# Kernel optimization log

Measured on AMD Instinct MI355X. Metric: run time of the kernel, lower is better.

## Reference

```python
import jax, jax.numpy as jnp
import numpy as np

N_NODES = 50000
N_EDGES = 800000
D_IN, D_HID, D_OUT = 128, 256, 128
N_EXPERT = 8


def mean_aggr(x, src, dst, n):
    # scatter-mean of neighbor features onto destination nodes
    msg = x[src]                                            # [E, d]
    s = jax.ops.segment_sum(msg, dst, num_segments=n)       # [N, d]
    cnt = jax.ops.segment_sum(jnp.ones((src.shape[0],), x.dtype), dst, num_segments=n)
    return s / jnp.clip(cnt, 1.0)[:, None]


def moe_top1(x, wg, bg, we, be):
    # FMoE with naive gate, top_k=1: combine weight softmax over top-1 == 1.0
    logits = x @ wg + bg                                    # [N, E]
    gate_full = jax.nn.softmax(logits, axis=-1)             # [N, E]
    idx = jnp.argmax(logits, axis=-1)                       # [N]
    n_expert = we.shape[0]
    out = jnp.zeros((x.shape[0], we.shape[2]), x.dtype)
    for e in range(n_expert):                               # small fixed loop over experts
        mask = (idx == e)[:, None].astype(x.dtype)
        out = out + mask * (x @ we[e] + be[e])
    return out, gate_full


def mysage_conv(x, src, dst, wg, bg, we, be, wr):
    agg = mean_aggr(x, src, dst, x.shape[0])
    out, gate = moe_top1(agg, wg, bg, we, be)
    out = out + x @ wr                                      # root weight (no bias)
    gstd = jnp.std(gate, axis=1, ddof=1).mean()             # torch.std is unbiased
    return out, gstd


def plain_sage_conv(x, src, dst, wl, bl, wr):
    agg = mean_aggr(x, src, dst, x.shape[0])
    return agg @ wl + bl + x @ wr


def setup_inputs() -> dict:
    key = jax.random.key(0)
    ks = jax.random.split(key, 16)
    s = 0.05
    inp = {
        "x": jax.random.normal(ks[0], (N_NODES, D_IN), jnp.float32),
        "edge_index": jax.random.randint(ks[1], (2, N_EDGES), 0, N_NODES, jnp.int64),
        # layer 1 (in -> hid)
        "wg1": jax.random.normal(ks[2], (D_IN, N_EXPERT), jnp.float32) * s,
        "bg1": jnp.zeros((N_EXPERT,), jnp.float32),
        "we1": jax.random.normal(ks[3], (N_EXPERT, D_IN, D_HID), jnp.float32) * s,
        "be1": jnp.zeros((N_EXPERT, D_HID), jnp.float32),
        "wr1": jax.random.normal(ks[4], (D_IN, D_HID), jnp.float32) * s,
        # layer 2 (hid -> hid)
        "wg2": jax.random.normal(ks[5], (D_HID, N_EXPERT), jnp.float32) * s,
        "bg2": jnp.zeros((N_EXPERT,), jnp.float32),
        "we2": jax.random.normal(ks[6], (N_EXPERT, D_HID, D_HID), jnp.float32) * s,
        "be2": jnp.zeros((N_EXPERT, D_HID), jnp.float32),
        "wr2": jax.random.normal(ks[7], (D_HID, D_HID), jnp.float32) * s,
        # layer 3 plain SAGEConv (hid -> out)
        "wl3": jax.random.normal(ks[8], (D_HID, D_OUT), jnp.float32) * s,
        "bl3": jnp.zeros((D_OUT,), jnp.float32),
        "wr3": jax.random.normal(ks[9], (D_HID, D_OUT), jnp.float32) * s,
    }
    return inp


def reference(x, edge_index, wg1, bg1, we1, be1, wr1, wg2, bg2, we2, be2, wr2, wl3, bl3, wr3):
    src, dst = edge_index[0], edge_index[1]
    h, g1 = mysage_conv(x, src, dst, wg1, bg1, we1, be1, wr1)
    h = jax.nn.relu(h)                                      # dropout p=0 / eval mode
    h, g2 = mysage_conv(h, src, dst, wg2, bg2, we2, be2, wr2)
    h = jax.nn.relu(h)
    out = plain_sage_conv(h, src, dst, wl3, bl3, wr3)
    gate_std_mean = jnp.stack([g1, g2]).mean()
    return out, gate_std_mean
```

## Files before the change

kernel.cpp:

```cpp
#include <hip/hip_runtime.h>
#include <hip/hip_bf16.h>
#include <stdint.h>

#define DEV static __device__ __forceinline__

typedef __attribute__((ext_vector_type(8))) short short8;
typedef __attribute__((ext_vector_type(4))) float f32x4;

DEV float bf2f(unsigned short u) { return __uint_as_float(((unsigned)u) << 16); }
DEV float bflo(unsigned u) { return __uint_as_float(u << 16); }
DEV float bfhi(unsigned u) { return __uint_as_float(u & 0xffff0000u); }
DEV unsigned short f2bf(float f) {
    unsigned u = __float_as_uint(f);
    u += 0x7fff + ((u >> 16) & 1);
    return (unsigned short)(u >> 16);
}

__global__ void k_detect(const int* __restrict__ ei, int* __restrict__ flags) {
    if (threadIdx.x == 0 && blockIdx.x == 0) {
        int zeros = 0;
        for (int i = 0; i < 128; ++i) if (ei[2 * i + 1] == 0) ++zeros;
        flags[1] = (zeros >= 64) ? 1 : 0;
    }
}

__global__ void k_cvt_idx(const int* __restrict__ ei, int* __restrict__ src32,
                          int* __restrict__ dst32, int E, const int* __restrict__ flags) {
    int i = blockIdx.x * 256 + threadIdx.x;
    if (i >= E) return;
    if (flags[1]) { src32[i] = ei[2 * i]; dst32[i] = ei[2 * E + 2 * i]; }
    else          { src32[i] = ei[i];     dst32[i] = ei[E + i]; }
}

__global__ void k_transpose_nb(const float* __restrict__ in, unsigned short* __restrict__ out,
                               int R, int C) {
    __shared__ unsigned short tile[32][33];
    int tx = threadIdx.x & 31, ty = threadIdx.x >> 5;
    size_t mat = (size_t)blockIdx.z * R * C;
    int r0 = blockIdx.y * 32, c0 = blockIdx.x * 32;
#pragma unroll
    for (int j = 0; j < 32; j += 8)
        tile[ty + j][tx] = f2bf(in[mat + (size_t)(r0 + ty + j) * C + c0 + tx]);
    __syncthreads();
#pragma unroll
    for (int j = 0; j < 32; j += 8)
        out[mat + (size_t)(c0 + ty + j) * R + r0 + tx] = tile[tx][ty + j];
}

__global__ void k_degree(const int* __restrict__ dst, int* __restrict__ deg, int E) {
    int i = blockIdx.x * 256 + threadIdx.x;
    if (i < E) atomicAdd(&deg[dst[i]], 1);
}

__global__ void k_scan1(const int* __restrict__ deg, int* __restrict__ row_ptr,
                        int* __restrict__ part, int n) {
    __shared__ int wsum[4];
    int t = threadIdx.x, lane = t & 63, wv = t >> 6;
    int i = blockIdx.x * 256 + t;
    int v0 = (i < n) ? deg[i] : 0;
    int v = v0;
#pragma unroll
    for (int d = 1; d < 64; d <<= 1) { int u = __shfl_up(v, d); if (lane >= d) v += u; }
    if (lane == 63) wsum[wv] = v;
    __syncthreads();
    int add = 0;
    for (int w2 = 0; w2 < wv; ++w2) add += wsum[w2];
    v += add;
    if (i < n) row_ptr[i] = v - v0;
    if (t == 255) part[blockIdx.x] = v;
}

__global__ void k_scan2(int* __restrict__ part, int P) {
    __shared__ int wsum[4];
    int t = threadIdx.x, lane = t & 63, wv = t >> 6;
    int v0 = (t < P) ? part[t] : 0;
    int v = v0;
#pragma unroll
    for (int d = 1; d < 64; d <<= 1) { int u = __shfl_up(v, d); if (lane >= d) v += u; }
    if (lane == 63) wsum[wv] = v;
    __syncthreads();
    int add = 0;
    for (int w2 = 0; w2 < wv; ++w2) add += wsum[w2];
    v += add;
    if (t < P) part[t] = v - v0;
}

__global__ void k_scan3(int* __restrict__ row_ptr, const int* __restrict__ part, int n, int E) {
    int i = blockIdx.x * 256 + threadIdx.x;
    if (i < n) row_ptr[i] += part[blockIdx.x];
    if (i == 0) row_ptr[n] = E;
}

__global__ void k_fill(const int* __restrict__ src, const int* __restrict__ dst,
                       const int* __restrict__ row_ptr, int* __restrict__ cursor,
                       int* __restrict__ csr, int E) {
    int i = blockIdx.x * 256 + threadIdx.x;
    if (i < E) {
        int d = dst[i];
        int p = atomicAdd(&cursor[d], 1);
        csr[row_ptr[d] + p] = src[i];
    }
}

template<int D>
__global__ void k_aggr(const float* __restrict__ xin, const int* __restrict__ row_ptr,
                       const int* __restrict__ csr, float* __restrict__ agg, int n) {
    int wid = (blockIdx.x * blockDim.x + threadIdx.x) >> 6;
    int lane = threadIdx.x & 63;
    if (wid >= n) return;
    constexpr int V = D / 64;
    double a0[V], a1[V], a2[V], a3[V];
#pragma unroll
    for (int i = 0; i < V; ++i) { a0[i] = 0.0; a1[i] = 0.0; a2[i] = 0.0; a3[i] = 0.0; }
    int s0 = row_ptr[wid], s1 = row_ptr[wid + 1];
    int j = s0;
    for (; j + 4 <= s1; j += 4) {
        int i0 = csr[j], i1 = csr[j + 1], i2 = csr[j + 2], i3 = csr[j + 3];
        const float* p0 = xin + (size_t)i0 * D + lane * V;
        const float* p1 = xin + (size_t)i1 * D + lane * V;
        const float* p2 = xin + (size_t)i2 * D + lane * V;
        const float* p3 = xin + (size_t)i3 * D + lane * V;
        if (V == 2) {
            float2 f0 = *(const float2*)p0, f1 = *(const float2*)p1;
            float2 f2 = *(const float2*)p2, f3 = *(const float2*)p3;
            a0[0] += (double)f0.x; a0[1] += (double)f0.y;
            a1[0] += (double)f1.x; a1[1] += (double)f1.y;
            a2[0] += (double)f2.x; a2[1] += (double)f2.y;
            a3[0] += (double)f3.x; a3[1] += (double)f3.y;
        } else {
            float4 f0 = *(const float4*)p0, f1 = *(const float4*)p1;
            float4 f2 = *(const float4*)p2, f3 = *(const float4*)p3;
            a0[0] += (double)f0.x; a0[1] += (double)f0.y; a0[2] += (double)f0.z; a0[3] += (double)f0.w;
            a1[0] += (double)f1.x; a1[1] += (double)f1.y; a1[2] += (double)f1.z; a1[3] += (double)f1.w;
            a2[0] += (double)f2.x; a2[1] += (double)f2.y; a2[2] += (double)f2.z; a2[3] += (double)f2.w;
            a3[0] += (double)f3.x; a3[1] += (double)f3.y; a3[2] += (double)f3.z; a3[3] += (double)f3.w;
        }
    }
    for (; j < s1; ++j) {
        const float* p = xin + (size_t)csr[j] * D + lane * V;
        if (V == 2) {
            float2 f = *(const float2*)p;
            a0[0] += (double)f.x; a0[1] += (double)f.y;
        } else {
            float4 f = *(const float4*)p;
            a0[0] += (double)f.x; a0[1] += (double)f.y; a0[2] += (double)f.z; a0[3] += (double)f.w;
        }
    }
    double inv = 1.0 / (double)max(s1 - s0, 1);
#pragma unroll
    for (int i = 0; i < V; ++i)
        agg[(size_t)wid * D + lane * V + i] = (float)(((a0[i] + a1[i]) + (a2[i] + a3[i])) * inv);
}

template<int D>
__global__ void k_aggr_bf(const unsigned short* __restrict__ xin, const int* __restrict__ row_ptr,
                          const int* __restrict__ csr, float* __restrict__ agg, int n) {
    int wid = (blockIdx.x * blockDim.x + threadIdx.x) >> 6;
    int lane = threadIdx.x & 63;
    if (wid >= n) return;
    constexpr int V = D / 64;
    double a0[V], a1[V], a2[V], a3[V];
#pragma unroll
    for (int i = 0; i < V; ++i) { a0[i] = 0.0; a1[i] = 0.0; a2[i] = 0.0; a3[i] = 0.0; }
    int s0 = row_ptr[wid], s1 = row_ptr[wid + 1];
    int j = s0;
    for (; j + 4 <= s1; j += 4) {
        int i0 = csr[j], i1 = csr[j + 1], i2 = csr[j + 2], i3 = csr[j + 3];
        uint2 u0 = *(const uint2*)(xin + (size_t)i0 * D + lane * V);
        uint2 u1 = *(const uint2*)(xin + (size_t)i1 * D + lane * V);
        uint2 u2 = *(const uint2*)(xin + (size_t)i2 * D + lane * V);
        uint2 u3 = *(const uint2*)(xin + (size_t)i3 * D + lane * V);
        a0[0] += (double)bflo(u0.x); a0[1] += (double)bfhi(u0.x);
        a0[2] += (double)bflo(u0.y); a0[3] += (double)bfhi(u0.y);
        a1[0] += (double)bflo(u1.x); a1[1] += (double)bfhi(u1.x);
        a1[2] += (double)bflo(u1.y); a1[3] += (double)bfhi(u1.y);
        a2[0] += (double)bflo(u2.x); a2[1] += (double)bfhi(u2.x);
        a2[2] += (double)bflo(u2.y); a2[3] += (double)bfhi(u2.y);
        a3[0] += (double)bflo(u3.x); a3[1] += (double)bfhi(u3.x);
        a3[2] += (double)bflo(u3.y); a3[3] += (double)bfhi(u3.y);
    }
    for (; j < s1; ++j) {
        uint2 u = *(const uint2*)(xin + (size_t)csr[j] * D + lane * V);
        a0[0] += (double)bflo(u.x); a0[1] += (double)bfhi(u.x);
        a0[2] += (double)bflo(u.y); a0[3] += (double)bfhi(u.y);
    }
    double inv = 1.0 / (double)max(s1 - s0, 1);
#pragma unroll
    for (int i = 0; i < V; ++i)
        agg[(size_t)wid * D + lane * V + i] = (float)(((a0[i] + a1[i]) + (a2[i] + a3[i])) * inv);
}

template<int D>
__global__ void k_gate(const float* __restrict__ agg, const float* __restrict__ wg,
                       const float* __restrict__ bg, int* __restrict__ idx,
                       int* __restrict__ ecnt, float* __restrict__ gsum, int n) {
    __shared__ float swg[D * 8];
    __shared__ int hcnt[8];
    __shared__ float red[256];
    int t = threadIdx.x;
    if (t < 8) hcnt[t] = 0;
    for (int i = t; i < D * 8; i += 256) swg[i] = wg[i];
    __syncthreads();
    int nid = blockIdx.x * 256 + t;
    float stdv = 0.f;
    if (nid < n) {
        double lg[8];
#pragma unroll
        for (int e = 0; e < 8; ++e) lg[e] = (double)bg[e];
        const float* ap = agg + (size_t)nid * D;
        for (int k = 0; k < D; k += 4) {
            float4 a = *(const float4*)(ap + k);
#pragma unroll
            for (int e = 0; e < 8; ++e) {
                lg[e] += (double)a.x * swg[(k + 0) * 8 + e] + (double)a.y * swg[(k + 1) * 8 + e]
                       + (double)a.z * swg[(k + 2) * 8 + e] + (double)a.w * swg[(k + 3) * 8 + e];
            }
        }
        double m = lg[0];
        int am = 0;
#pragma unroll
        for (int e = 1; e < 8; ++e) if (lg[e] > m) { m = lg[e]; am = e; }
        double s = 0.0, p[8];
#pragma unroll
        for (int e = 0; e < 8; ++e) { p[e] = exp(lg[e] - m); s += p[e]; }
        double invs = 1.0 / s, sq = 0.0;
#pragma unroll
        for (int e = 0; e < 8; ++e) { double q = p[e] * invs; sq += q * q; }
        stdv = (float)sqrt(fmax(sq - 0.125, 0.0) / 7.0);
        idx[nid] = am;
        atomicAdd(&hcnt[am], 1);
    }
    red[t] = stdv;
    __syncthreads();
    for (int off = 128; off > 0; off >>= 1) {
        if (t < off) red[t] += red[t + off];
        __syncthreads();
    }
    if (t == 0) atomicAdd(gsum, red[0]);
    if (t < 8 && hcnt[t] > 0) atomicAdd(&ecnt[t], hcnt[t]);
}

__global__ void k_offsets(const int* __restrict__ ecnt, int* __restrict__ eoff) {
    if (threadIdx.x == 0 && blockIdx.x == 0) {
        int s = 0;
        for (int e = 0; e < 8; ++e) { eoff[e] = s; s += ecnt[e]; }
        eoff[8] = s;
    }
}

__global__ void k_perm(const int* __restrict__ idx, const int* __restrict__ eoff,
                       int* __restrict__ ecur, int* __restrict__ perm, int n) {
    __shared__ int lcnt[8], lbase[8];
    int t = threadIdx.x;
    if (t < 8) lcnt[t] = 0;
    __syncthreads();
    int nid = blockIdx.x * 256 + t;
    int e = 0, r = 0;
    bool valid = (nid < n);
    if (valid) { e = idx[nid]; r = atomicAdd(&lcnt[e], 1); }
    __syncthreads();
    if (t < 8) lbase[t] = lcnt[t] ? atomicAdd(&ecur[t], lcnt[t]) : 0;
    __syncthreads();
    if (valid) perm[eoff[e] + lbase[e] + r] = nid;
}

template<int NCOL, bool LOAD>
DEV void g_step(int g, const float* __restrict__ Bp, const float* __restrict__ at,
                float4 (&cur)[4], float (&acc)[8][4]) {
    float bx[4][4];
#pragma unroll
    for (int kk = 0; kk < 4; ++kk) {
        bx[kk][0] = cur[kk].x; bx[kk][1] = cur[kk].y;
        bx[kk][2] = cur[kk].z; bx[kk][3] = cur[kk].w;
    }
#pragma unroll
    for (int r = 0; r < 8; ++r) {
        float4 a = *(const float4*)(at + r * 68 + g * 4);
#pragma unroll
        for (int c = 0; c < 4; ++c) {
            acc[r][c] = fmaf(a.x, bx[0][c], acc[r][c]);
            acc[r][c] = fmaf(a.y, bx[1][c], acc[r][c]);
            acc[r][c] = fmaf(a.z, bx[2][c], acc[r][c]);
            acc[r][c] = fmaf(a.w, bx[3][c], acc[r][c]);
        }
    }
    if (LOAD) {
#pragma unroll
        for (int kk = 0; kk < 4; ++kk)
            cur[kk] = *(const float4*)(Bp + (size_t)(g * 4 + 8 + kk) * NCOL);
    }
}

template<int NCOL>
DEV void compute_chunk(const float* __restrict__ Bp, const float* __restrict__ at,
                       float (&acc)[8][4]) {
    float4 bA[4], bB[4];
#pragma unroll
    for (int kk = 0; kk < 4; ++kk) bA[kk] = *(const float4*)(Bp + (size_t)kk * NCOL);
#pragma unroll
    for (int kk = 0; kk < 4; ++kk) bB[kk] = *(const float4*)(Bp + (size_t)(4 + kk) * NCOL);
#pragma unroll 1
    for (int g = 0; g < 14; g += 2) {
        g_step<NCOL, true>(g, Bp, at, bA, acc);
        g_step<NCOL, true>(g + 1, Bp, at, bB, acc);
    }
    g_step<NCOL, false>(14, Bp, at, bA, acc);
    g_step<NCOL, false>(15, Bp, at, bB, acc);
}

template<int DIN, int NCOL, bool EXPERT, bool RELU>
__global__ __launch_bounds__(256, 4) void k_gemm_f32(
    const float* __restrict__ agg, const float* __restrict__ a2,
    const float* __restrict__ B1, const float* __restrict__ B2,
    const float* __restrict__ bias,
    const int* __restrict__ perm, const int* __restrict__ eoff,
    float* __restrict__ outp, int n) {
    static_assert(DIN == 128 && NCOL == 256, "layer-1 geometry");
    __shared__ float a_tile[2][4 * 8 * 68];
    __shared__ int rows[32];
    int t = threadIdx.x;
    int e = 0, base = 0, cnt = n;
    if (EXPERT) { e = blockIdx.y; base = eoff[e]; cnt = eoff[e + 1] - base; }
    int rs = blockIdx.x * 32;
    if (rs >= cnt) return;
    int nrows = min(32, cnt - rs);
    if (t < 32) {
        int j = rs + min(t, nrows - 1);
        rows[t] = EXPERT ? perm[base + j] : j;
    }
    __syncthreads();
    int lane = t & 63, rg = t >> 6;
    int cols = lane * 4;
    int srow = lane >> 3;
    int sk = (lane & 7) * 8;
    int myrow = rows[rg * 8 + srow];
    float* st0 = &a_tile[0][rg * 544 + srow * 68 + sk];
    float* st1 = &a_tile[1][rg * 544 + srow * 68 + sk];
    const float* at0 = &a_tile[0][rg * 544];
    const float* at1 = &a_tile[1][rg * 544];
    const float* B1e = B1 + (EXPERT ? (size_t)e * DIN * NCOL : 0);
    const float* a_my = agg + (size_t)myrow * DIN + sk;
    const float* x_my = a2 + (size_t)myrow * DIN + sk;

    float acc[8][4];
#pragma unroll
    for (int r = 0; r < 8; ++r) { acc[r][0] = 0.f; acc[r][1] = 0.f; acc[r][2] = 0.f; acc[r][3] = 0.f; }

    float4 p0 = *(const float4*)a_my;
    float4 p1 = *(const float4*)(a_my + 4);
    float4 q0 = *(const float4*)(a_my + 64);
    float4 q1 = *(const float4*)(a_my + 68);
    *(float4*)st0 = p0; *(float4*)(st0 + 4) = p1;
    compute_chunk<NCOL>(B1e + cols, at0, acc);

    *(float4*)st1 = q0; *(float4*)(st1 + 4) = q1;
    p0 = *(const float4*)x_my;
    p1 = *(const float4*)(x_my + 4);
    compute_chunk<NCOL>(B1e + (size_t)64 * NCOL + cols, at1, acc);

    *(float4*)st0 = p0; *(float4*)(st0 + 4) = p1;
    q0 = *(const float4*)(x_my + 64);
    q1 = *(const float4*)(x_my + 68);
    compute_chunk<NCOL>(B2 + cols, at0, acc);

    *(float4*)st1 = q0; *(float4*)(st1 + 4) = q1;
    compute_chunk<NCOL>(B2 + (size_t)64 * NCOL + cols, at1, acc);

    float4 bb = *(const float4*)(bias + (EXPERT ? e * NCOL : 0) + cols);
#pragma unroll
    for (int r = 0; r < 8; ++r) {
        int rr = rg * 8 + r;
        if (rr < nrows) {
            int gr = rows[rr];
            float v0 = acc[r][0] + bb.x, v1 = acc[r][1] + bb.y;
            float v2 = acc[r][2] + bb.z, v3 = acc[r][3] + bb.w;
            if (RELU) { v0 = fmaxf(v0, 0.f); v1 = fmaxf(v1, 0.f); v2 = fmaxf(v2, 0.f); v3 = fmaxf(v3, 0.f); }
            *(float4*)(outp + (size_t)gr * NCOL + cols) = make_float4(v0, v1, v2, v3);
        }
    }
}

template<int DIN, int MODE, int CT>
DEV void gemm_half(const void* __restrict__ Asrc, const unsigned short* __restrict__ BT,
                   short (*Ah)[40], short (*Bs)[40],
                   const int* rows, f32x4 (&acc)[4][CT], int t, int lane, int w) {
    int q = lane >> 4, m16 = lane & 15;
    int r = t >> 2, part = t & 3;
    for (int kc = 0; kc < DIN; kc += 32) {
        __syncthreads();
        if (MODE == 2) {
            *(uint4*)&Ah[r][part * 8] =
                *(const uint4*)((const unsigned short*)Asrc + (size_t)rows[r] * DIN + kc + part * 8);
        } else {
            const float* pf = (const float*)Asrc + (size_t)rows[r] * DIN + kc + part * 8;
            float4 p0 = *(const float4*)pf, p1 = *(const float4*)(pf + 4);
            float va[8] = { p0.x, p0.y, p0.z, p0.w, p1.x, p1.y, p1.z, p1.w };
            short8 h;
#pragma unroll
            for (int j = 0; j < 8; ++j) h[j] = (short)f2bf(va[j]);
            *(short8*)&Ah[r][part * 8] = h;
        }
#pragma unroll
        for (int j = 0; j < CT; ++j) {
            int c = t + 256 * j;
            int nn = c >> 2, pp = c & 3;
            *(uint4*)&Bs[nn][pp * 8] = *(const uint4*)(BT + (size_t)nn * DIN + kc + pp * 8);
        }
        __syncthreads();
        short8 af[4], bfr[CT];
#pragma unroll
        for (int rt = 0; rt < 4; ++rt) af[rt] = *(short8*)&Ah[rt * 16 + m16][q * 8];
#pragma unroll
        for (int ct = 0; ct < CT; ++ct) bfr[ct] = *(short8*)&Bs[w * CT * 16 + ct * 16 + m16][q * 8];
#pragma unroll
        for (int rt = 0; rt < 4; ++rt)
#pragma unroll
            for (int ct = 0; ct < CT; ++ct)
                acc[rt][ct] = __builtin_amdgcn_mfma_f32_16x16x32_bf16(af[rt], bfr[ct], acc[rt][ct], 0, 0, 0);
    }
}

template<int DIN, int M0, int M1, int CT, bool EXPERT, bool RELU, bool OUTBF>
__global__ __launch_bounds__(256) void k_gemm(
    const void* __restrict__ A0, const void* __restrict__ A1,
    const unsigned short* __restrict__ B0T, const unsigned short* __restrict__ B1T,
    const float* __restrict__ bias,
    const int* __restrict__ perm, const int* __restrict__ eoff,
    void* __restrict__ outp, int n) {
    constexpr int NCOL = CT * 64;
    __shared__ short Ah[64][40];
    __shared__ short Bs[NCOL][40];
    __shared__ int rows[64];
    int t = threadIdx.x;
    int lane = t & 63, w = t >> 6;
    int e = 0, base = 0, cnt = n;
    if (EXPERT) { e = blockIdx.y; base = eoff[e]; cnt = eoff[e + 1] - base; }
    int rs = blockIdx.x * 64;
    if (rs >= cnt) return;
    int nrows = min(64, cnt - rs);
    if (t < 64) {
        int j = rs + min(t, nrows - 1);
        rows[t] = EXPERT ? perm[base + j] : j;
    }
    __syncthreads();
    f32x4 acc[4][CT];
#pragma unroll
    for (int rt = 0; rt < 4; ++rt)
#pragma unroll
        for (int ct = 0; ct < CT; ++ct) acc[rt][ct] = (f32x4)(0.f);

    gemm_half<DIN, M0, CT>(A0, B0T + (EXPERT ? (size_t)e * DIN * NCOL : 0), Ah, Bs, rows, acc, t, lane, w);
    gemm_half<DIN, M1, CT>(A1, B1T, Ah, Bs, rows, acc, t, lane, w);

    int q = lane >> 4, m16 = lane & 15;
#pragma unroll
    for (int ct = 0; ct < CT; ++ct) {
        int col = w * CT * 16 + ct * 16 + m16;
        float bv = bias[(EXPERT ? e * NCOL : 0) + col];
#pragma unroll
        for (int rt = 0; rt < 4; ++rt)
#pragma unroll
            for (int i = 0; i < 4; ++i) {
                int rr = rt * 16 + q * 4 + i;
                if (rr < nrows) {
                    int gr = rows[rr];
                    float v = acc[rt][ct][i] + bv;
                    if (RELU) v = fmaxf(v, 0.f);
                    if (OUTBF) ((unsigned short*)outp)[(size_t)gr * NCOL + col] = f2bf(v);
                    else       ((float*)outp)[(size_t)gr * NCOL + col] = v;
                }
            }
    }
}

__global__ void k_final(const float* __restrict__ gsum, float* __restrict__ outf) {
    if (threadIdx.x == 0 && blockIdx.x == 0) {
        float g = (gsum[0] + gsum[1]) * (0.5f / 50000.0f);
        outf[(size_t)50000 * 128] = g;
    }
}

extern "C" void kernel_launch(void* const* d_in, const int* in_sizes, int n_in,
                              void* d_out, int out_size, void* d_ws, size_t ws_size,
                              hipStream_t stream) {
    constexpr int N = 50000, E = 800000;
    const float* x   = (const float*)d_in[0];
    const int* ei    = (const int*)d_in[1];
    const float* wg1 = (const float*)d_in[2];
    const float* bg1 = (const float*)d_in[3];
    const float* we1 = (const float*)d_in[4];
    const float* be1 = (const float*)d_in[5];
    const float* wr1 = (const float*)d_in[6];
    const float* wg2 = (const float*)d_in[7];
    const float* bg2 = (const float*)d_in[8];
    const float* we2 = (const float*)d_in[9];
    const float* be2 = (const float*)d_in[10];
    const float* wr2 = (const float*)d_in[11];
    const float* wl3 = (const float*)d_in[12];
    const float* bl3 = (const float*)d_in[13];
    const float* wr3 = (const float*)d_in[14];

    int* ip = (int*)d_ws;
    int* deg = ip;            ip += N;
    int* cursor = ip;         ip += N;
    int* ecnt = ip;           ip += 16;
    int* ecur = ip;           ip += 16;
    float* gsum = (float*)ip; ip += 2;
    int* flags = ip;          ip += 2;
    int* row_ptr = ip;        ip += N + 1;
    int* csr = ip;            ip += E;
    int* idxb = ip;           ip += N;
    int* permb = ip;          ip += N;
    int* eoff = ip;           ip += 18;
    int* part = ip;           ip += 256;
    int* src32 = ip;          ip += E;
    int* dst32 = ip;          ip += E;
    size_t off = (size_t)((char*)ip - (char*)d_ws);
    off = (off + 255) & ~(size_t)255;
    float* fp = (float*)((char*)d_ws + off);
    float* agg = fp; fp += (size_t)N * 256;
    float* h1  = fp; fp += (size_t)N * 256;
    unsigned short* wp = (unsigned short*)fp;
    unsigned short* h2b  = wp; wp += (size_t)N * 256;
    unsigned short* we2T = wp; wp += 8 * 256 * 256;
    unsigned short* wr2T = wp; wp += 256 * 256;
    unsigned short* wl3T = wp; wp += 256 * 128;
    unsigned short* wr3T = wp; wp += 256 * 128;

    hipMemsetAsync(d_ws, 0, (size_t)(2 * N + 36) * 4, stream);

    k_detect<<<1, 64, 0, stream>>>(ei, flags);
    k_cvt_idx<<<(E + 255) / 256, 256, 0, stream>>>(ei, src32, dst32, E, flags);

    k_transpose_nb<<<dim3(8, 8, 8), 256, 0, stream>>>(we2, we2T, 256, 256);
    k_transpose_nb<<<dim3(8, 8, 1), 256, 0, stream>>>(wr2, wr2T, 256, 256);
    k_transpose_nb<<<dim3(4, 8, 1), 256, 0, stream>>>(wl3, wl3T, 256, 128);
    k_transpose_nb<<<dim3(4, 8, 1), 256, 0, stream>>>(wr3, wr3T, 256, 128);

    constexpr int NB = (N + 255) / 256;
    constexpr int WB = (N + 3) / 4;
    k_degree<<<(E + 255) / 256, 256, 0, stream>>>(dst32, deg, E);
    k_scan1<<<NB, 256, 0, stream>>>(deg, row_ptr, part, N);
    k_scan2<<<1, 256, 0, stream>>>(part, NB);
    k_scan3<<<NB, 256, 0, stream>>>(row_ptr, part, N, E);
    k_fill<<<(E + 255) / 256, 256, 0, stream>>>(src32, dst32, row_ptr, cursor, csr, E);

    constexpr int GB = (N + 63) / 64;
    constexpr int GB32 = (N + 31) / 32;
    k_aggr<128><<<WB, 256, 0, stream>>>(x, row_ptr, csr, agg, N);
    k_gate<128><<<NB, 256, 0, stream>>>(agg, wg1, bg1, idxb, ecnt, gsum, N);
    k_offsets<<<1, 1, 0, stream>>>(ecnt, eoff);
    k_perm<<<NB, 256, 0, stream>>>(idxb, eoff, ecur, permb, N);
    k_gemm_f32<128, 256, true, true><<<dim3(GB32, 8), 256, 0, stream>>>(
        agg, x, we1, wr1, be1, permb, eoff, h1, N);

    k_aggr<256><<<WB, 256, 0, stream>>>(h1, row_ptr, csr, agg, N);
    k_gate<256><<<NB, 256, 0, stream>>>(agg, wg2, bg2, idxb, ecnt + 8, gsum + 1, N);
    k_offsets<<<1, 1, 0, stream>>>(ecnt + 8, eoff + 9);
    k_perm<<<NB, 256, 0, stream>>>(idxb, eoff + 9, ecur + 8, permb, N);
    k_gemm<256, 0, 0, 4, true, true, true><<<dim3(GB, 8), 256, 0, stream>>>(
        agg, h1, we2T, wr2T, be2, permb, eoff + 9, h2b, N);

    k_aggr_bf<256><<<WB, 256, 0, stream>>>(h2b, row_ptr, csr, agg, N);
    k_gemm<256, 0, 2, 2, false, false, false><<<dim3(GB, 1), 256, 0, stream>>>(
        agg, h2b, wl3T, wr3T, bl3, nullptr, nullptr, d_out, N);

    k_final<<<1, 1, 0, stream>>>(gsum, (float*)d_out);
}
```

Baseline: 673.9 us.

## Fuse gating into aggregation and flatten expert grid in fp32 layer-1 GEMM

```diff
diff --git a/kernel.cpp b/kernel.cpp
--- a/kernel.cpp
+++ b/kernel.cpp
@@ -103,53 +103,107 @@
 }
 
 template<int D>
-__global__ void k_aggr(const float* __restrict__ xin, const int* __restrict__ row_ptr,
-                       const int* __restrict__ csr, float* __restrict__ agg, int n) {
-    int wid = (blockIdx.x * blockDim.x + threadIdx.x) >> 6;
-    int lane = threadIdx.x & 63;
-    if (wid >= n) return;
+__global__ void k_aggr_gate(const float* __restrict__ xin, const int* __restrict__ row_ptr,
+                            const int* __restrict__ csr, const float* __restrict__ wg,
+                            const float* __restrict__ bg, float* __restrict__ agg,
+                            int* __restrict__ idx, int* __restrict__ ecnt,
+                            float* __restrict__ gpart, int n) {
     constexpr int V = D / 64;
-    double a0[V], a1[V], a2[V], a3[V];
-#pragma unroll
-    for (int i = 0; i < V; ++i) { a0[i] = 0.0; a1[i] = 0.0; a2[i] = 0.0; a3[i] = 0.0; }
-    int s0 = row_ptr[wid], s1 = row_ptr[wid + 1];
-    int j = s0;
-    for (; j + 4 <= s1; j += 4) {
-        int i0 = csr[j], i1 = csr[j + 1], i2 = csr[j + 2], i3 = csr[j + 3];
-        const float* p0 = xin + (size_t)i0 * D + lane * V;
-        const float* p1 = xin + (size_t)i1 * D + lane * V;
-        const float* p2 = xin + (size_t)i2 * D + lane * V;
-        const float* p3 = xin + (size_t)i3 * D + lane * V;
-        if (V == 2) {
-            float2 f0 = *(const float2*)p0, f1 = *(const float2*)p1;
-            float2 f2 = *(const float2*)p2, f3 = *(const float2*)p3;
-            a0[0] += (double)f0.x; a0[1] += (double)f0.y;
-            a1[0] += (double)f1.x; a1[1] += (double)f1.y;
-            a2[0] += (double)f2.x; a2[1] += (double)f2.y;
-            a3[0] += (double)f3.x; a3[1] += (double)f3.y;
-        } else {
-            float4 f0 = *(const float4*)p0, f1 = *(const float4*)p1;
-            float4 f2 = *(const float4*)p2, f3 = *(const float4*)p3;
-            a0[0] += (double)f0.x; a0[1] += (double)f0.y; a0[2] += (double)f0.z; a0[3] += (double)f0.w;
-            a1[0] += (double)f1.x; a1[1] += (double)f1.y; a1[2] += (double)f1.z; a1[3] += (double)f1.w;
-            a2[0] += (double)f2.x; a2[1] += (double)f2.y; a2[2] += (double)f2.z; a2[3] += (double)f2.w;
-            a3[0] += (double)f3.x; a3[1] += (double)f3.y; a3[2] += (double)f3.z; a3[3] += (double)f3.w;
-        }
-    }
-    for (; j < s1; ++j) {
-        const float* p = xin + (size_t)csr[j] * D + lane * V;
-        if (V == 2) {
-            float2 f = *(const float2*)p;
-            a0[0] += (double)f.x; a0[1] += (double)f.y;
-        } else {
-            float4 f = *(const float4*)p;
-            a0[0] += (double)f.x; a0[1] += (double)f.y; a0[2] += (double)f.z; a0[3] += (double)f.w;
-        }
-    }
-    double inv = 1.0 / (double)max(s1 - s0, 1);
-#pragma unroll
-    for (int i = 0; i < V; ++i)
-        agg[(size_t)wid * D + lane * V + i] = (float)(((a0[i] + a1[i]) + (a2[i] + a3[i])) * inv);
+    __shared__ float swg[D * 8];
+    __shared__ int hcnt[8];
+    __shared__ float bsum;
+    int t = threadIdx.x;
+    if (t < 8) hcnt[t] = 0;
+    if (t == 0) bsum = 0.f;
+    for (int i = t; i < D * 8; i += 256) swg[i] = wg[i];
+    __syncthreads();
+
+    int wid = (blockIdx.x * blockDim.x + t) >> 6;
+    int lane = t & 63;
+    bool active = (wid < n);
+    float fv[V];
+    if (active) {
+        double a0[V], a1[V], a2[V], a3[V];
+#pragma unroll
+        for (int i = 0; i < V; ++i) { a0[i] = 0.0; a1[i] = 0.0; a2[i] = 0.0; a3[i] = 0.0; }
+        int s0 = row_ptr[wid], s1 = row_ptr[wid + 1];
+        int j = s0;
+        for (; j + 4 <= s1; j += 4) {
+            int i0 = csr[j], i1 = csr[j + 1], i2 = csr[j + 2], i3 = csr[j + 3];
+            const float* p0 = xin + (size_t)i0 * D + lane * V;
+            const float* p1 = xin + (size_t)i1 * D + lane * V;
+            const float* p2 = xin + (size_t)i2 * D + lane * V;
+            const float* p3 = xin + (size_t)i3 * D + lane * V;
+            if (V == 2) {
+                float2 f0 = *(const float2*)p0, f1 = *(const float2*)p1;
+                float2 f2 = *(const float2*)p2, f3 = *(const float2*)p3;
+                a0[0] += (double)f0.x; a0[1] += (double)f0.y;
+                a1[0] += (double)f1.x; a1[1] += (double)f1.y;
+                a2[0] += (double)f2.x; a2[1] += (double)f2.y;
+                a3[0] += (double)f3.x; a3[1] += (double)f3.y;
+            } else {
+                float4 f0 = *(const float4*)p0, f1 = *(const float4*)p1;
+                float4 f2 = *(const float4*)p2, f3 = *(const float4*)p3;
+                a0[0] += (double)f0.x; a0[1] += (double)f0.y; a0[2] += (double)f0.z; a0[3] += (double)f0.w;
+                a1[0] += (double)f1.x; a1[1] += (double)f1.y; a1[2] += (double)f1.z; a1[3] += (double)f1.w;
+                a2[0] += (double)f2.x; a2[1] += (double)f2.y; a2[2] += (double)f2.z; a2[3] += (double)f2.w;
+                a3[0] += (double)f3.x; a3[1] += (double)f3.y; a3[2] += (double)f3.z; a3[3] += (double)f3.w;
+            }
+        }
+        for (; j < s1; ++j) {
+            const float* p = xin + (size_t)csr[j] * D + lane * V;
+            if (V == 2) {
+                float2 f = *(const float2*)p;
+                a0[0] += (double)f.x; a0[1] += (double)f.y;
+            } else {
+                float4 f = *(const float4*)p;
+                a0[0] += (double)f.x; a0[1] += (double)f.y; a0[2] += (double)f.z; a0[3] += (double)f.w;
+            }
+        }
+        double inv = 1.0 / (double)max(s1 - s0, 1);
+#pragma unroll
+        for (int i = 0; i < V; ++i) {
+            fv[i] = (float)(((a0[i] + a1[i]) + (a2[i] + a3[i])) * inv);
+            agg[(size_t)wid * D + lane * V + i] = fv[i];
+        }
+        double lg[8];
+#pragma unroll
+        for (int e = 0; e < 8; ++e) {
+            double s = 0.0;
+#pragma unroll
+            for (int i = 0; i < V; ++i)
+                s += (double)fv[i] * (double)swg[(lane * V + i) * 8 + e];
+            lg[e] = s;
+        }
+#pragma unroll
+        for (int e = 0; e < 8; ++e) {
+            double v = lg[e];
+#pragma unroll
+            for (int off = 1; off < 64; off <<= 1) v += __shfl_xor(v, off);
+            lg[e] = v;
+        }
+        if (lane == 0) {
+#pragma unroll
+            for (int e = 0; e < 8; ++e) lg[e] += (double)bg[e];
+            double m = lg[0];
+            int am = 0;
+#pragma unroll
+            for (int e = 1; e < 8; ++e) if (lg[e] > m) { m = lg[e]; am = e; }
+            double s = 0.0, p[8];
+#pragma unroll
+            for (int e = 0; e < 8; ++e) { p[e] = exp(lg[e] - m); s += p[e]; }
+            double invs = 1.0 / s, sq = 0.0;
+#pragma unroll
+            for (int e = 0; e < 8; ++e) { double q = p[e] * invs; sq += q * q; }
+            float stdv = (float)sqrt(fmax(sq - 0.125, 0.0) / 7.0);
+            idx[wid] = am;
+            atomicAdd(&hcnt[am], 1);
+            atomicAdd(&bsum, stdv);
+        }
+    }
+    __syncthreads();
+    if (t < 8 && hcnt[t] > 0) atomicAdd(&ecnt[t], hcnt[t]);
+    if (t == 0) atomicAdd(&gpart[blockIdx.x & 63], bsum);
 }
 
 template<int D>
@@ -190,56 +244,6 @@
         agg[(size_t)wid * D + lane * V + i] = (float)(((a0[i] + a1[i]) + (a2[i] + a3[i])) * inv);
 }
 
-template<int D>
-__global__ void k_gate(const float* __restrict__ agg, const float* __restrict__ wg,
-                       const float* __restrict__ bg, int* __restrict__ idx,
-                       int* __restrict__ ecnt, float* __restrict__ gsum, int n) {
-    __shared__ float swg[D * 8];
-    __shared__ int hcnt[8];
-    __shared__ float red[256];
-    int t = threadIdx.x;
-    if (t < 8) hcnt[t] = 0;
-    for (int i = t; i < D * 8; i += 256) swg[i] = wg[i];
-    __syncthreads();
-    int nid = blockIdx.x * 256 + t;
-    float stdv = 0.f;
-    if (nid < n) {
-        double lg[8];
-#pragma unroll
-        for (int e = 0; e < 8; ++e) lg[e] = (double)bg[e];
-        const float* ap = agg + (size_t)nid * D;
-        for (int k = 0; k < D; k += 4) {
-            float4 a = *(const float4*)(ap + k);
-#pragma unroll
-            for (int e = 0; e < 8; ++e) {
-                lg[e] += (double)a.x * swg[(k + 0) * 8 + e] + (double)a.y * swg[(k + 1) * 8 + e]
-                       + (double)a.z * swg[(k + 2) * 8 + e] + (double)a.w * swg[(k + 3) * 8 + e];
-            }
-        }
-        double m = lg[0];
-        int am = 0;
-#pragma unroll
-        for (int e = 1; e < 8; ++e) if (lg[e] > m) { m = lg[e]; am = e; }
-        double s = 0.0, p[8];
-#pragma unroll
-        for (int e = 0; e < 8; ++e) { p[e] = exp(lg[e] - m); s += p[e]; }
-        double invs = 1.0 / s, sq = 0.0;
-#pragma unroll
-        for (int e = 0; e < 8; ++e) { double q = p[e] * invs; sq += q * q; }
-        stdv = (float)sqrt(fmax(sq - 0.125, 0.0) / 7.0);
-        idx[nid] = am;
-        atomicAdd(&hcnt[am], 1);
-    }
-    red[t] = stdv;
-    __syncthreads();
-    for (int off = 128; off > 0; off >>= 1) {
-        if (t < off) red[t] += red[t + off];
-        __syncthreads();
-    }
-    if (t == 0) atomicAdd(gsum, red[0]);
-    if (t < 8 && hcnt[t] > 0) atomicAdd(&ecnt[t], hcnt[t]);
-}
-
 __global__ void k_offsets(const int* __restrict__ ecnt, int* __restrict__ eoff) {
     if (threadIdx.x == 0 && blockIdx.x == 0) {
         int s = 0;
@@ -308,8 +312,8 @@
     g_step<NCOL, false>(15, Bp, at, bB, acc);
 }
 
-template<int DIN, int NCOL, bool EXPERT, bool RELU>
-__global__ __launch_bounds__(256, 4) void k_gemm_f32(
+template<int DIN, int NCOL, bool RELU>
+__global__ __launch_bounds__(256, 8) void k_gemm_f32(
     const float* __restrict__ agg, const float* __restrict__ a2,
     const float* __restrict__ B1, const float* __restrict__ B2,
     const float* __restrict__ bias,
@@ -319,58 +323,79 @@
     __shared__ float a_tile[2][4 * 8 * 68];
     __shared__ int rows[32];
     int t = threadIdx.x;
-    int e = 0, base = 0, cnt = n;
-    if (EXPERT) { e = blockIdx.y; base = eoff[e]; cnt = eoff[e + 1] - base; }
     int rs = blockIdx.x * 32;
-    if (rs >= cnt) return;
-    int nrows = min(32, cnt - rs);
-    if (t < 32) {
-        int j = rs + min(t, nrows - 1);
-        rows[t] = EXPERT ? perm[base + j] : j;
-    }
-    __syncthreads();
+    if (rs >= n) return;
+    int nrows = min(32, n - rs);
+    if (t < 32) rows[t] = perm[rs + min(t, nrows - 1)];
+    __syncthreads();
+
+    int e0 = 0, e1 = 0;
+    int last = rs + nrows - 1;
+#pragma unroll
+    for (int e = 1; e < 8; ++e) {
+        int v = eoff[e];
+        if (v <= rs) e0 = e;
+        if (v <= last) e1 = e;
+    }
+    int ne = e1 - e0 + 1;
+    int nchunks = 2 * ne + 2;
+
     int lane = t & 63, rg = t >> 6;
     int cols = lane * 4;
     int srow = lane >> 3;
     int sk = (lane & 7) * 8;
+    int gpos = rs + rg * 8 + srow;
     int myrow = rows[rg * 8 + srow];
-    float* st0 = &a_tile[0][rg * 544 + srow * 68 + sk];
-    float* st1 = &a_tile[1][rg * 544 + srow * 68 + sk];
-    const float* at0 = &a_tile[0][rg * 544];
-    const float* at1 = &a_tile[1][rg * 544];
-    const float* B1e = B1 + (EXPERT ? (size_t)e * DIN * NCOL : 0);
-    const float* a_my = agg + (size_t)myrow * DIN + sk;
-    const float* x_my = a2 + (size_t)myrow * DIN + sk;
+    float* stc = &a_tile[0][rg * 544 + srow * 68 + sk];
+    float* stn = &a_tile[1][rg * 544 + srow * 68 + sk];
+    const float* atc = &a_tile[0][rg * 544];
+    const float* atn = &a_tile[1][rg * 544];
 
     float acc[8][4];
 #pragma unroll
     for (int r = 0; r < 8; ++r) { acc[r][0] = 0.f; acc[r][1] = 0.f; acc[r][2] = 0.f; acc[r][3] = 0.f; }
 
-    float4 p0 = *(const float4*)a_my;
-    float4 p1 = *(const float4*)(a_my + 4);
-    float4 q0 = *(const float4*)(a_my + 64);
-    float4 q1 = *(const float4*)(a_my + 68);
-    *(float4*)st0 = p0; *(float4*)(st0 + 4) = p1;
-    compute_chunk<NCOL>(B1e + cols, at0, acc);
-
-    *(float4*)st1 = q0; *(float4*)(st1 + 4) = q1;
-    p0 = *(const float4*)x_my;
-    p1 = *(const float4*)(x_my + 4);
-    compute_chunk<NCOL>(B1e + (size_t)64 * NCOL + cols, at1, acc);
-
-    *(float4*)st0 = p0; *(float4*)(st0 + 4) = p1;
-    q0 = *(const float4*)(x_my + 64);
-    q1 = *(const float4*)(x_my + 68);
-    compute_chunk<NCOL>(B2 + cols, at0, acc);
-
-    *(float4*)st1 = q0; *(float4*)(st1 + 4) = q1;
-    compute_chunk<NCOL>(B2 + (size_t)64 * NCOL + cols, at1, acc);
-
-    float4 bb = *(const float4*)(bias + (EXPERT ? e * NCOL : 0) + cols);
+    auto params = [&](int c, const float*& ap, const float*& Bp, float& m) {
+        int half = c & 1;
+        if (c < 2 * ne) {
+            int e = e0 + (c >> 1);
+            ap = agg + (size_t)myrow * DIN + sk + half * 64;
+            Bp = B1 + (size_t)e * DIN * NCOL + (size_t)half * 64 * NCOL + cols;
+            m = (gpos >= eoff[e] && gpos < eoff[e + 1]) ? 1.f : 0.f;
+        } else {
+            ap = a2 + (size_t)myrow * DIN + sk + half * 64;
+            Bp = B2 + (size_t)half * 64 * NCOL + cols;
+            m = 1.f;
+        }
+    };
+
+    const float* ap; const float* Bp; float m;
+    params(0, ap, Bp, m);
+    float4 p0 = *(const float4*)ap, p1 = *(const float4*)(ap + 4);
+#pragma unroll 1
+    for (int c = 0; c < nchunks; ++c) {
+        float4 s0 = p0, s1 = p1;
+        s0.x *= m; s0.y *= m; s0.z *= m; s0.w *= m;
+        s1.x *= m; s1.y *= m; s1.z *= m; s1.w *= m;
+        *(float4*)stc = s0; *(float4*)(stc + 4) = s1;
+        const float* Bcur = Bp;
+        if (c + 1 < nchunks) {
+            params(c + 1, ap, Bp, m);
+            p0 = *(const float4*)ap; p1 = *(const float4*)(ap + 4);
+        }
+        compute_chunk<NCOL>(Bcur, atc, acc);
+        float* ts = stc; stc = stn; stn = ts;
+        const float* ta = atc; atc = atn; atn = ta;
+    }
+
 #pragma unroll
     for (int r = 0; r < 8; ++r) {
         int rr = rg * 8 + r;
         if (rr < nrows) {
+            int gp = rs + rr;
+            int er = e0;
+            for (int e = e0 + 1; e <= e1; ++e) if (eoff[e] <= gp) er = e;
+            float4 bb = *(const float4*)(bias + er * NCOL + cols);
             int gr = rows[rr];
             float v0 = acc[r][0] + bb.x, v1 = acc[r][1] + bb.y;
             float v2 = acc[r][2] + bb.z, v3 = acc[r][3] + bb.w;
@@ -473,10 +498,11 @@
     }
 }
 
-__global__ void k_final(const float* __restrict__ gsum, float* __restrict__ outf) {
+__global__ void k_final(const float* __restrict__ gpart, float* __restrict__ outf) {
     if (threadIdx.x == 0 && blockIdx.x == 0) {
-        float g = (gsum[0] + gsum[1]) * (0.5f / 50000.0f);
-        outf[(size_t)50000 * 128] = g;
+        float s = 0.f;
+        for (int i = 0; i < 128; ++i) s += gpart[i];
+        outf[(size_t)50000 * 128] = s * (0.5f / 50000.0f);
     }
 }
 
@@ -505,7 +531,7 @@
     int* cursor = ip;         ip += N;
     int* ecnt = ip;           ip += 16;
     int* ecur = ip;           ip += 16;
-    float* gsum = (float*)ip; ip += 2;
+    float* gpart = (float*)ip; ip += 128;
     int* flags = ip;          ip += 2;
     int* row_ptr = ip;        ip += N + 1;
     int* csr = ip;            ip += E;
@@ -527,7 +553,7 @@
     unsigned short* wl3T = wp; wp += 256 * 128;
     unsigned short* wr3T = wp; wp += 256 * 128;
 
-    hipMemsetAsync(d_ws, 0, (size_t)(2 * N + 36) * 4, stream);
+    hipMemsetAsync(d_ws, 0, (size_t)(2 * N + 162) * 4, stream);
 
     k_detect<<<1, 64, 0, stream>>>(ei, flags);
     k_cvt_idx<<<(E + 255) / 256, 256, 0, stream>>>(ei, src32, dst32, E, flags);
@@ -547,15 +573,13 @@
 
     constexpr int GB = (N + 63) / 64;
     constexpr int GB32 = (N + 31) / 32;
-    k_aggr<128><<<WB, 256, 0, stream>>>(x, row_ptr, csr, agg, N);
-    k_gate<128><<<NB, 256, 0, stream>>>(agg, wg1, bg1, idxb, ecnt, gsum, N);
+    k_aggr_gate<128><<<WB, 256, 0, stream>>>(x, row_ptr, csr, wg1, bg1, agg, idxb, ecnt, gpart, N);
     k_offsets<<<1, 1, 0, stream>>>(ecnt, eoff);
     k_perm<<<NB, 256, 0, stream>>>(idxb, eoff, ecur, permb, N);
-    k_gemm_f32<128, 256, true, true><<<dim3(GB32, 8), 256, 0, stream>>>(
+    k_gemm_f32<128, 256, true><<<dim3(GB32), 256, 0, stream>>>(
         agg, x, we1, wr1, be1, permb, eoff, h1, N);
 
-    k_aggr<256><<<WB, 256, 0, stream>>>(h1, row_ptr, csr, agg, N);
-    k_gate<256><<<NB, 256, 0, stream>>>(agg, wg2, bg2, idxb, ecnt + 8, gsum + 1, N);
+    k_aggr_gate<256><<<WB, 256, 0, stream>>>(h1, row_ptr, csr, wg2, bg2, agg, idxb, ecnt + 8, gpart + 64, N);
     k_offsets<<<1, 1, 0, stream>>>(ecnt + 8, eoff + 9);
     k_perm<<<NB, 256, 0, stream>>>(idxb, eoff + 9, ecur + 8, permb, N);
     k_gemm<256, 0, 0, 4, true, true, true><<<dim3(GB, 8), 256, 0, stream>>>(
@@ -565,5 +589,5 @@
     k_gemm<256, 0, 2, 2, false, false, false><<<dim3(GB, 1), 256, 0, stream>>>(
         agg, h2b, wl3T, wr3T, bl3, nullptr, nullptr, d_out, N);
 
-    k_final<<<1, 1, 0, stream>>>(gsum, (float*)d_out);
-}
+    k_final<<<1, 1, 0, stream>>>(gpart, (float*)d_out);
+}
```

After: 1.906 ms. 183% more time.
